# Kernel tuning notes

Measured on AMD Instinct MI355X. Metric: run time of the kernel, lower is better.

Reference implementation:

```python
import jax, jax.numpy as jnp
import numpy as np

N, T, K, V, E = 64, 256, 64, 32000, 100


def setup_inputs() -> dict:
    key = jax.random.key(0)
    ks = jax.random.split(key, 7)
    x = jax.random.randint(ks[0], (N, T), 0, V)
    emb_weight = jax.random.normal(ks[1], (V, E), dtype=jnp.float32)
    # trans: Linear(E, K*K, bias=False), weight uniform(-1,1)
    W_trans = jax.random.uniform(ks[2], (K * K, E), minval=-1.0, maxval=1.0, dtype=jnp.float32)
    # start: Linear(1, K)
    start_w = jax.random.normal(ks[3], (K, 1), dtype=jnp.float32) * 0.1
    start_b = jax.random.normal(ks[4], (K,), dtype=jnp.float32) * 0.1
    # emb_cluster: Embedding(K, K)
    emb_cluster_w = jax.random.normal(ks[5], (K, K), dtype=jnp.float32)
    # vocab: Linear(K, V, bias=False), weight uniform(-1,1)
    vocab_w = jax.random.uniform(ks[6], (V, K), minval=-1.0, maxval=1.0, dtype=jnp.float32)
    return {"x": x, "emb_weight": emb_weight, "W_trans": W_trans,
            "start_w": start_w, "start_b": start_b,
            "emb_cluster_w": emb_cluster_w, "vocab_w": vocab_w}


def reference(x, emb_weight, W_trans, start_w, start_b, emb_cluster_w, vocab_w):
    n, t = x.shape
    k = emb_cluster_w.shape[0]
    # word embeddings used to condition transitions at steps 0..T-2
    xe = emb_weight[x[:, :-1]]                                   # [N,T-1,E]
    # transition log-probs: log_softmax over destination state
    tran = jax.nn.log_softmax(
        jnp.einsum('nte,ce->ntc', xe, W_trans).reshape(n, t - 1, k, k), axis=-1)
    # emission log-probs per cluster: E[k, v]
    Elog = jax.nn.log_softmax(emb_cluster_w @ vocab_w.T, axis=-1)  # [K,V]
    emit = Elog.T[x[:, 1:]]                                       # [N,T-1,K]
    # initial alpha: log_softmax(start(ones)) expanded over batch
    alpha0 = jax.nn.log_softmax(start_w[:, 0] + start_b)           # [K]
    alpha0 = jnp.broadcast_to(alpha0[None, :], (n, k))
    tran_t = jnp.moveaxis(tran, 1, 0)   # [T-1,N,K,K]
    emit_t = jnp.moveaxis(emit, 1, 0)   # [T-1,N,K]

    def step(alpha, te):
        tr, em = te
        # logsumexp over previous state j: alpha[n,j] + tr[n,j,k]
        a = jax.scipy.special.logsumexp(alpha[:, :, None] + tr, axis=1) + em
        return a, None

    alpha, _ = jax.lax.scan(step, alpha0, (tran_t, emit_t))
    return -jnp.mean(jax.scipy.special.logsumexp(alpha, axis=1))
```

## Files before the change

kernel.cpp:

```cpp
#include <hip/hip_runtime.h>
#include <hip/hip_bf16.h>
#include <stdint.h>

#define NT 16320
#define NTPAD 16384
#define KDIM 128
#define NCOLS 4096
#define NSEQ 64
#define TSTEPS 255
#define VOCAB 32000
#define EDIM 100
#define CHUNKS 32
#define CLEN 8

typedef __attribute__((ext_vector_type(8))) short s8v;
typedef __attribute__((ext_vector_type(4))) float f4v;

__device__ __forceinline__ float bflo(uint32_t u) { return __uint_as_float(u << 16); }
__device__ __forceinline__ float bfhi(uint32_t u) { return __uint_as_float(u & 0xffff0000u); }

__device__ __forceinline__ void load_lds16(const void* g, void* l) {
    __builtin_amdgcn_global_load_lds(
        (const __attribute__((address_space(1))) void*)(uintptr_t)g,
        (__attribute__((address_space(3))) void*)(uintptr_t)l,
        16, 0, 0);
}

__global__ __launch_bounds__(256) void prep_dk(const int* __restrict__ x,
                                               const float* __restrict__ emb,
                                               const float* __restrict__ Wt,
                                               const float* __restrict__ ec,
                                               const float* __restrict__ vw,
                                               __hip_bfloat16* __restrict__ A,
                                               __hip_bfloat16* __restrict__ B,
                                               float* __restrict__ partials) {
    int bid = blockIdx.x;
    int tid = threadIdx.x;
    if (bid < 1280) {
        int rloc = tid >> 4, q = tid & 15;
        int b = bid * 16 + rloc;
        int c0 = q * 8;
        float vals[8] = {0.f, 0.f, 0.f, 0.f, 0.f, 0.f, 0.f, 0.f};
        __hip_bfloat16* dst;
        if (b < NTPAD) {
            if (b < NT) {
                int n = b / TSTEPS;
                int t = b - n * TSTEPS;
                int tok = x[n * 256 + t];
                const float* er = emb + (size_t)tok * EDIM;
#pragma unroll
                for (int i = 0; i < 8; ++i) { int e = c0 + i; if (e < EDIM) vals[i] = er[e]; }
            }
            dst = A + (size_t)b * KDIM + c0;
        } else {
            int cc = b - NTPAD;
            const float* wr = Wt + (size_t)cc * EDIM;
#pragma unroll
            for (int i = 0; i < 8; ++i) { int e = c0 + i; if (e < EDIM) vals[i] = wr[e]; }
            dst = B + (size_t)cc * KDIM + c0;
        }
        union { __hip_bfloat16 h[8]; uint4 u; } pk;
#pragma unroll
        for (int i = 0; i < 8; ++i) pk.h[i] = __float2bfloat16(vals[i]);
        *(uint4*)dst = pk.u;
    } else {
        int db = bid - 1280;
        int wave = tid >> 6, lane = tid & 63;
        float er[64];
        {
            const float4* ecv = (const float4*)(ec + (size_t)lane * 64);
#pragma unroll
            for (int i = 0; i < 16; ++i) {
                float4 v = ecv[i];
                er[4 * i] = v.x; er[4 * i + 1] = v.y; er[4 * i + 2] = v.z; er[4 * i + 3] = v.w;
            }
        }
        int v0 = db * 125;
        float m = -1e30f, s = 0.f;
        for (int v = v0 + wave; v < v0 + 125; v += 4) {
            int vu = __builtin_amdgcn_readfirstlane(v);
            const float* row = vw + (size_t)vu * 64;
            float acc = 0.f;
#pragma unroll
            for (int e = 0; e < 64; ++e) acc += er[e] * row[e];
            float nm = fmaxf(m, acc);
            s = s * __expf(m - nm) + __expf(acc - nm);
            m = nm;
        }
        __shared__ float pm[4][64], ps[4][64];
        pm[wave][lane] = m; ps[wave][lane] = s;
        __syncthreads();
        if (tid < 64) {
            float M = pm[0][tid], Ssum = ps[0][tid];
#pragma unroll
            for (int w = 1; w < 4; ++w) {
                float m2 = pm[w][tid], s2 = ps[w][tid];
                float nm = fmaxf(M, m2);
                Ssum = Ssum * __expf(M - nm) + s2 * __expf(m2 - nm);
                M = nm;
            }
            partials[(db * 64 + tid) * 2]     = M;
            partials[(db * 64 + tid) * 2 + 1] = Ssum;
        }
    }
}

__global__ __launch_bounds__(256) void dreduce(const float* __restrict__ partials,
                                               float* __restrict__ d) {
    __shared__ float pm[4][64], ps[4][64];
    int k = threadIdx.x & 63, part = threadIdx.x >> 6;
    float M = -1e30f, S = 0.f;
    for (int b = part; b < 256; b += 4) {
        float m2 = partials[(b * 64 + k) * 2];
        float s2 = partials[(b * 64 + k) * 2 + 1];
        float nm = fmaxf(M, m2);
        S = S * __expf(M - nm) + s2 * __expf(m2 - nm);
        M = nm;
    }
    pm[part][k] = M; ps[part][k] = S;
    __syncthreads();
    if (threadIdx.x < 64) {
        float Mm = pm[0][k], Ss = ps[0][k];
#pragma unroll
        for (int w = 1; w < 4; ++w) {
            float m2 = pm[w][k], s2 = ps[w][k];
            float nm = fmaxf(Mm, m2);
            Ss = Ss * __expf(Mm - nm) + s2 * __expf(m2 - nm);
            Mm = nm;
        }
        d[k] = Mm + __logf(Ss);
    }
}

__global__ __launch_bounds__(256) void emit_kern(const int* __restrict__ x,
                                                 const float* __restrict__ ec,
                                                 const float* __restrict__ vw,
                                                 const float* __restrict__ d,
                                                 __hip_bfloat16* __restrict__ emB) {
    int tid = threadIdx.x;
    int wave = tid >> 6, lane = tid & 63;
    float er[64];
    {
        const float4* ecv = (const float4*)(ec + (size_t)lane * 64);
#pragma unroll
        for (int i = 0; i < 16; ++i) {
            float4 v = ecv[i];
            er[4 * i] = v.x; er[4 * i + 1] = v.y; er[4 * i + 2] = v.z; er[4 * i + 3] = v.w;
        }
    }
    float dj = d[lane];
    int j = lane;
    int pos = ((j >> 2) & 3) * 16 + ((j >> 4) & 3) * 4 + (j & 3);
    int nt0 = blockIdx.x * 16 + wave * 4;
#pragma unroll
    for (int s = 0; s < 4; ++s) {
        int nt = nt0 + s;
        int n = nt / TSTEPS;
        int t = nt - n * TSTEPS;
        int tok = x[n * 256 + t + 1];
        tok = __builtin_amdgcn_readfirstlane(tok);
        const float* row = vw + (size_t)tok * 64;
        float acc = 0.f;
#pragma unroll
        for (int e = 0; e < 64; ++e) acc += er[e] * row[e];
        emB[(size_t)nt * 64 + pos] = __float2bfloat16(__expf(acc - dj));
    }
}

__global__ __launch_bounds__(256) void gemm_kern(const __hip_bfloat16* __restrict__ A,
                                                 const __hip_bfloat16* __restrict__ B,
                                                 const __hip_bfloat16* __restrict__ emB,
                                                 __hip_bfloat16* __restrict__ Eg) {
    int mblk = blockIdx.x;
    int nblk = blockIdx.y;
    int tid = threadIdx.x, wave = tid >> 6, lane = tid & 63;

    __shared__ __align__(16) char smem[65536];
    char* sA = smem;
    char* sB = smem + 32768;

    {
        int r0 = wave * 32;
        int l16 = lane & 15;
        int rsub = lane >> 4;
#pragma unroll
        for (int g = 0; g < 8; ++g) {
            int r = r0 + g * 4 + rsub;
            int chunk = l16 ^ (r & 7);
            const char* gp = (const char*)(A + (size_t)(mblk * 128 + r) * KDIM) + chunk * 16;
            load_lds16(gp, sA + (r0 + g * 4) * 256);
        }
#pragma unroll
        for (int g = 0; g < 8; ++g) {
            int c = r0 + g * 4 + rsub;
            int chunk = l16 ^ (c & 7);
            const char* gp = (const char*)(B + (size_t)(nblk * 128 + c) * KDIM) + chunk * 16;
            load_lds16(gp, sB + (r0 + g * 4) * 256);
        }
    }
    __syncthreads();

    int wc = (wave >> 1) * 64, wm = (wave & 1) * 64;
    int l15 = lane & 15, g4 = lane >> 4;
    f4v acc[4][4] = {};
#pragma unroll
    for (int k32 = 0; k32 < 4; ++k32) {
        s8v af[4], bf[4];
#pragma unroll
        for (int jt = 0; jt < 4; ++jt) {
            int r = wc + jt * 16 + l15;
            int chunk = (k32 * 4 + g4) ^ (r & 7);
            af[jt] = *(const s8v*)(sB + r * 256 + chunk * 16);
        }
#pragma unroll
        for (int mt = 0; mt < 4; ++mt) {
            int r = wm + mt * 16 + l15;
            int chunk = (k32 * 4 + g4) ^ (r & 7);
            bf[mt] = *(const s8v*)(sA + r * 256 + chunk * 16);
        }
#pragma unroll
        for (int jt = 0; jt < 4; ++jt)
#pragma unroll
            for (int mt = 0; mt < 4; ++mt)
                acc[jt][mt] = __builtin_amdgcn_mfma_f32_16x16x32_bf16(af[jt], bf[mt], acc[jt][mt], 0, 0, 0);
    }
    __syncthreads();

    char* sW = smem;
    const char* emb8 = (const char*)emB;
#pragma unroll
    for (int mt = 0; mt < 4; ++mt) {
        int mrow = wm + mt * 16 + l15;
        int mglob = mblk * 128 + mrow;
        float v[16];
#pragma unroll
        for (int jt = 0; jt < 4; ++jt)
#pragma unroll
            for (int rr = 0; rr < 4; ++rr) v[jt * 4 + rr] = acc[jt][mt][rr];
        float mx = v[0];
#pragma unroll
        for (int k = 1; k < 16; ++k) mx = fmaxf(mx, v[k]);
        mx = fmaxf(mx, __shfl_xor(mx, 16, 64));
        mx = fmaxf(mx, __shfl_xor(mx, 32, 64));
        float ex[16], sg = 0.f;
#pragma unroll
        for (int k = 0; k < 16; ++k) { ex[k] = __expf(v[k] - mx); sg += ex[k]; }
        sg += __shfl_xor(sg, 16, 64);
        sg += __shfl_xor(sg, 32, 64);
        float inv = 1.0f / sg;
        uint4 e0 = *(const uint4*)(emb8 + (size_t)mglob * 128 + g4 * 32);
        uint4 e1 = *(const uint4*)(emb8 + (size_t)mglob * 128 + g4 * 32 + 16);
        float em[16];
        {
            const uint32_t* w0 = (const uint32_t*)&e0;
            const uint32_t* w1 = (const uint32_t*)&e1;
#pragma unroll
            for (int i = 0; i < 4; ++i) {
                em[2 * i] = bflo(w0[i]);     em[2 * i + 1] = bfhi(w0[i]);
                em[8 + 2 * i] = bflo(w1[i]); em[8 + 2 * i + 1] = bfhi(w1[i]);
            }
        }
#pragma unroll
        for (int jt = 0; jt < 4; ++jt) {
            union { __hip_bfloat16 h[4]; uint2 u; } pk;
#pragma unroll
            for (int rr = 0; rr < 4; ++rr)
                pk.h[rr] = __float2bfloat16(ex[jt * 4 + rr] * inv * em[jt * 4 + rr]);
            *(uint2*)(sW + mrow * 272 + (wc + jt * 16 + g4 * 4) * 2) = pk.u;
        }
    }
    __syncthreads();

    {
        int rloc = tid >> 3;
        int q = tid & 7;
#pragma unroll
        for (int rp = 0; rp < 4; ++rp) {
            int row = rp * 32 + rloc;
            char* dst = (char*)Eg + (size_t)(mblk * 128 + row) * 8192 + nblk * 256;
            const char* src = sW + row * 272;
            *(uint4*)(dst + q * 16)       = *(const uint4*)(src + q * 16);
            *(uint4*)(dst + 128 + q * 16) = *(const uint4*)(src + 128 + q * 16);
        }
    }
}

__global__ __launch_bounds__(64) void chunk_kern(const __hip_bfloat16* __restrict__ Eg,
                                                 __hip_bfloat16* __restrict__ Gout,
                                                 float* __restrict__ Rout) {
    int lane = threadIdx.x;
    int l15 = lane & 15, g4 = lane >> 4;
    int id = blockIdx.x;
    int n = id >> 5;
    int c = id & 31;
    int base_m = n * TSTEPS + c * CLEN;
    int len = (c == 31) ? 7 : 8;

    __shared__ __align__(16) char sGT[64 * 144];

    {
        uint4 z = {0, 0, 0, 0};
#pragma unroll
        for (int i = 0; i < 8; ++i) *(uint4*)(sGT + lane * 144 + i * 16) = z;
        *(uint16_t*)(sGT + lane * 144 + lane * 2) = 0x3F80;
    }

    const char* Ebase = (const char*)Eg;
    uint4 pf[4][2];
    {
        const char* tp = Ebase + (size_t)(base_m + len - 1) * 8192;
#pragma unroll
        for (int at = 0; at < 4; ++at)
#pragma unroll
            for (int kk = 0; kk < 2; ++kk)
                pf[at][kk] = *(const uint4*)(tp + (at * 16 + l15) * 128 + kk * 64 + g4 * 16);
    }

    float rlog[4] = {0.f, 0.f, 0.f, 0.f};

    for (int tl = len - 1; tl >= 0; --tl) {
        uint4 af[4][2];
#pragma unroll
        for (int at = 0; at < 4; ++at) { af[at][0] = pf[at][0]; af[at][1] = pf[at][1]; }
        if (tl > 0) {
            const char* tp = Ebase + (size_t)(base_m + tl - 1) * 8192;
#pragma unroll
            for (int at = 0; at < 4; ++at)
#pragma unroll
                for (int kk = 0; kk < 2; ++kk)
                    pf[at][kk] = *(const uint4*)(tp + (at * 16 + l15) * 128 + kk * 64 + g4 * 16);
        }

        f4v acc[4][4] = {};
#pragma unroll
        for (int kk = 0; kk < 2; ++kk) {
#pragma unroll
            for (int ct = 0; ct < 4; ++ct) {
                s8v b = *(const s8v*)(sGT + (ct * 16 + l15) * 144 + kk * 64 + g4 * 16);
#pragma unroll
                for (int at = 0; at < 4; ++at)
                    acc[at][ct] = __builtin_amdgcn_mfma_f32_16x16x32_bf16(
                        *(const s8v*)&af[at][kk], b, acc[at][ct], 0, 0, 0);
            }
        }

#pragma unroll
        for (int ct = 0; ct < 4; ++ct) {
            float mx = acc[0][ct][0];
#pragma unroll
            for (int at = 0; at < 4; ++at)
#pragma unroll
                for (int rr = 0; rr < 4; ++rr) mx = fmaxf(mx, acc[at][ct][rr]);
            mx = fmaxf(mx, __shfl_xor(mx, 16, 64));
            mx = fmaxf(mx, __shfl_xor(mx, 32, 64));
            mx = fmaxf(mx, 1e-38f);
            rlog[ct] += __logf(mx);
            float inv = 1.0f / mx;
            int col = ct * 16 + l15;
#pragma unroll
            for (int at = 0; at < 4; ++at) {
                union { __hip_bfloat16 h[4]; uint2 u; } pk;
#pragma unroll
                for (int rr = 0; rr < 4; ++rr)
                    pk.h[rr] = __float2bfloat16(acc[at][ct][rr] * inv);
                *(uint2*)(sGT + col * 144 + at * 32 + g4 * 8) = pk.u;
            }
        }
    }

    {
        char* go = (char*)(Gout + (size_t)id * 4096 + lane * 64);
#pragma unroll
        for (int i = 0; i < 8; ++i)
            *(uint4*)(go + i * 16) = *(const uint4*)(sGT + lane * 144 + i * 16);
    }
    if (g4 == 0)
#pragma unroll
        for (int ct = 0; ct < 4; ++ct)
            Rout[(size_t)id * 64 + ct * 16 + l15] = rlog[ct];
}

__global__ __launch_bounds__(64) void combine_kern(const __hip_bfloat16* __restrict__ G,
                                                   const float* __restrict__ R,
                                                   const float* __restrict__ sw,
                                                   const float* __restrict__ sb,
                                                   float* __restrict__ out) {
    int n = blockIdx.x;
    int lane = threadIdx.x;
    __shared__ __align__(16) float sV[64];

    float alpha;
    {
        float v = sw[lane] + sb[lane];
        float m = v;
#pragma unroll
        for (int off = 1; off < 64; off <<= 1) m = fmaxf(m, __shfl_xor(m, off, 64));
        float s = __expf(v - m);
#pragma unroll
        for (int off = 1; off < 64; off <<= 1) s += __shfl_xor(s, off, 64);
        alpha = v - (m + __logf(s));
    }

    const char* Gb = (const char*)(G + (size_t)n * CHUNKS * 4096) + lane * 128;
    const float* Rb = R + (size_t)n * CHUNKS * 64 + lane;

    uint4 pf[8];
#pragma unroll
    for (int i = 0; i < 8; ++i) pf[i] = *(const uint4*)(Gb + i * 16);
    float rpf = Rb[0];

    for (int c = 0; c < CHUNKS; ++c) {
        uint4 cur[8];
#pragma unroll
        for (int i = 0; i < 8; ++i) cur[i] = pf[i];
        float rc = rpf;
        if (c + 1 < CHUNKS) {
            const char* gn = Gb + (size_t)(c + 1) * 8192;
#pragma unroll
            for (int i = 0; i < 8; ++i) pf[i] = *(const uint4*)(gn + i * 16);
            rpf = Rb[(c + 1) * 64];
        }

        float m = alpha;
#pragma unroll
        for (int off = 1; off < 64; off <<= 1) m = fmaxf(m, __shfl_xor(m, off, 64));
        sV[lane] = __expf(alpha - m);
        float acc = 0.f;
        const float4* sv4 = (const float4*)sV;
#pragma unroll
        for (int i = 0; i < 8; ++i) {
            const uint32_t* gw = (const uint32_t*)&cur[i];
            float4 va = sv4[2 * i], vb = sv4[2 * i + 1];
            acc += va.x * bflo(gw[0]) + va.y * bfhi(gw[0]);
            acc += va.z * bflo(gw[1]) + va.w * bfhi(gw[1]);
            acc += vb.x * bflo(gw[2]) + vb.y * bfhi(gw[2]);
            acc += vb.z * bflo(gw[3]) + vb.w * bfhi(gw[3]);
        }
        alpha = m + __logf(fmaxf(acc, 1e-38f)) + rc;
    }

    {
        float m = alpha;
#pragma unroll
        for (int off = 1; off < 64; off <<= 1) m = fmaxf(m, __shfl_xor(m, off, 64));
        float s = __expf(alpha - m);
#pragma unroll
        for (int off = 1; off < 64; off <<= 1) s += __shfl_xor(s, off, 64);
        if (lane == 0) atomicAdd(out, -(m + __logf(s)) * (1.0f / 64.0f));
    }
}

extern "C" void kernel_launch(void* const* d_in, const int* in_sizes, int n_in,
                              void* d_out, int out_size, void* d_ws, size_t ws_size,
                              hipStream_t stream) {
    const int*   x   = (const int*)d_in[0];
    const float* emb = (const float*)d_in[1];
    const float* Wt  = (const float*)d_in[2];
    const float* sw  = (const float*)d_in[3];
    const float* sb  = (const float*)d_in[4];
    const float* ec  = (const float*)d_in[5];
    const float* vw  = (const float*)d_in[6];
    float* out = (float*)d_out;
    char* ws = (char*)d_ws;

    __hip_bfloat16* Eg  = (__hip_bfloat16*)ws;
    __hip_bfloat16* A   = (__hip_bfloat16*)(ws + 134217728ull);
    __hip_bfloat16* B   = (__hip_bfloat16*)(ws + 138412032ull);
    __hip_bfloat16* emB = (__hip_bfloat16*)(ws + 139460608ull);
    float* dvec         = (float*)(ws + 141557760ull);
    float* partials     = (float*)(ws + 141558784ull);
    __hip_bfloat16* Gc  = (__hip_bfloat16*)(ws + 134217728ull);
    float* Rc           = (float*)(ws + 150994944ull);

    hipMemsetAsync(out, 0, sizeof(float), stream);

    prep_dk<<<1536, 256, 0, stream>>>(x, emb, Wt, ec, vw, A, B, partials);
    dreduce<<<1, 256, 0, stream>>>(partials, dvec);
    emit_kern<<<NT / 16, 256, 0, stream>>>(x, ec, vw, dvec, emB);
    gemm_kern<<<dim3(NTPAD / 128, NCOLS / 128), 256, 0, stream>>>(A, B, emB, Eg);
    chunk_kern<<<NSEQ * CHUNKS, 64, 0, stream>>>(Eg, Gc, Rc);
    combine_kern<<<NSEQ, 64, 0, stream>>>(Gc, Rc, sw, sb, out);
}
```

Baseline: 231.0 us.

## Narrow GEMM N-tile to 64 and rebalance scan chunks to 17x15

The GEMM now computes 128x64 output tiles instead of 128x128. This cuts LDS use and accumulator registers and doubles the number of blocks, which should raise occupancy. Stores for padded rows past NT are skipped. The chunked scan now splits each 255-step sequence into 17 chunks of exactly 15 steps instead of 32 chunks of 8, so every chunk has the same length and the combine stage has fewer chunks to merge, at the cost of fewer, longer chunk blocks. The Gc and Rc workspace buffers are moved to new offsets so they no longer overlap A and B.

```diff
diff --git a/kernel.cpp b/kernel.cpp
--- a/kernel.cpp
+++ b/kernel.cpp
@@ -10,8 +10,8 @@
 #define TSTEPS 255
 #define VOCAB 32000
 #define EDIM 100
-#define CHUNKS 32
-#define CLEN 8
+#define CHUNKS 17
+#define CLEN 15
 
 typedef __attribute__((ext_vector_type(8))) short s8v;
 typedef __attribute__((ext_vector_type(4))) float f4v;
@@ -175,45 +175,44 @@
     int nblk = blockIdx.y;
     int tid = threadIdx.x, wave = tid >> 6, lane = tid & 63;
 
-    __shared__ __align__(16) char smem[65536];
+    __shared__ __align__(16) char smem[49152];
     char* sA = smem;
     char* sB = smem + 32768;
 
     {
-        int r0 = wave * 32;
         int l16 = lane & 15;
         int rsub = lane >> 4;
 #pragma unroll
         for (int g = 0; g < 8; ++g) {
-            int r = r0 + g * 4 + rsub;
+            int r = wave * 32 + g * 4 + rsub;
             int chunk = l16 ^ (r & 7);
             const char* gp = (const char*)(A + (size_t)(mblk * 128 + r) * KDIM) + chunk * 16;
-            load_lds16(gp, sA + (r0 + g * 4) * 256);
-        }
-#pragma unroll
-        for (int g = 0; g < 8; ++g) {
-            int c = r0 + g * 4 + rsub;
-            int chunk = l16 ^ (c & 7);
-            const char* gp = (const char*)(B + (size_t)(nblk * 128 + c) * KDIM) + chunk * 16;
-            load_lds16(gp, sB + (r0 + g * 4) * 256);
+            load_lds16(gp, sA + (wave * 32 + g * 4) * 256);
+        }
+#pragma unroll
+        for (int g = 0; g < 4; ++g) {
+            int r = wave * 16 + g * 4 + rsub;
+            int chunk = l16 ^ (r & 7);
+            const char* gp = (const char*)(B + (size_t)(nblk * 64 + r) * KDIM) + chunk * 16;
+            load_lds16(gp, sB + (wave * 16 + g * 4) * 256);
         }
     }
     __syncthreads();
 
-    int wc = (wave >> 1) * 64, wm = (wave & 1) * 64;
+    int wm = wave * 32;
     int l15 = lane & 15, g4 = lane >> 4;
-    f4v acc[4][4] = {};
+    f4v acc[4][2] = {};
 #pragma unroll
     for (int k32 = 0; k32 < 4; ++k32) {
-        s8v af[4], bf[4];
+        s8v af[4], bf[2];
 #pragma unroll
         for (int jt = 0; jt < 4; ++jt) {
-            int r = wc + jt * 16 + l15;
+            int r = jt * 16 + l15;
             int chunk = (k32 * 4 + g4) ^ (r & 7);
             af[jt] = *(const s8v*)(sB + r * 256 + chunk * 16);
         }
 #pragma unroll
-        for (int mt = 0; mt < 4; ++mt) {
+        for (int mt = 0; mt < 2; ++mt) {
             int r = wm + mt * 16 + l15;
             int chunk = (k32 * 4 + g4) ^ (r & 7);
             bf[mt] = *(const s8v*)(sA + r * 256 + chunk * 16);
@@ -221,7 +220,7 @@
 #pragma unroll
         for (int jt = 0; jt < 4; ++jt)
 #pragma unroll
-            for (int mt = 0; mt < 4; ++mt)
+            for (int mt = 0; mt < 2; ++mt)
                 acc[jt][mt] = __builtin_amdgcn_mfma_f32_16x16x32_bf16(af[jt], bf[mt], acc[jt][mt], 0, 0, 0);
     }
     __syncthreads();
@@ -229,7 +228,7 @@
     char* sW = smem;
     const char* emb8 = (const char*)emB;
 #pragma unroll
-    for (int mt = 0; mt < 4; ++mt) {
+    for (int mt = 0; mt < 2; ++mt) {
         int mrow = wm + mt * 16 + l15;
         int mglob = mblk * 128 + mrow;
         float v[16];
@@ -266,21 +265,22 @@
 #pragma unroll
             for (int rr = 0; rr < 4; ++rr)
                 pk.h[rr] = __float2bfloat16(ex[jt * 4 + rr] * inv * em[jt * 4 + rr]);
-            *(uint2*)(sW + mrow * 272 + (wc + jt * 16 + g4 * 4) * 2) = pk.u;
+            *(uint2*)(sW + mrow * 136 + (jt * 16 + g4 * 4) * 2) = pk.u;
         }
     }
     __syncthreads();
 
     {
-        int rloc = tid >> 3;
-        int q = tid & 7;
+        int rloc = lane >> 3;
+        int q = lane & 7;
 #pragma unroll
         for (int rp = 0; rp < 4; ++rp) {
-            int row = rp * 32 + rloc;
-            char* dst = (char*)Eg + (size_t)(mblk * 128 + row) * 8192 + nblk * 256;
-            const char* src = sW + row * 272;
-            *(uint4*)(dst + q * 16)       = *(const uint4*)(src + q * 16);
-            *(uint4*)(dst + 128 + q * 16) = *(const uint4*)(src + 128 + q * 16);
+            int row = wave * 32 + rp * 8 + rloc;
+            int m = mblk * 128 + row;
+            if (m < NT) {
+                char* dst = (char*)Eg + (size_t)m * 8192 + nblk * 128;
+                *(uint4*)(dst + q * 16) = *(const uint4*)(sW + row * 136 + q * 16);
+            }
         }
     }
 }
@@ -291,10 +291,9 @@
     int lane = threadIdx.x;
     int l15 = lane & 15, g4 = lane >> 4;
     int id = blockIdx.x;
-    int n = id >> 5;
-    int c = id & 31;
+    int n = (id * 3856) >> 16;
+    int c = id - n * 17;
     int base_m = n * TSTEPS + c * CLEN;
-    int len = (c == 31) ? 7 : 8;
 
     __shared__ __align__(16) char sGT[64 * 144];
 
@@ -308,7 +307,7 @@
     const char* Ebase = (const char*)Eg;
     uint4 pf[4][2];
     {
-        const char* tp = Ebase + (size_t)(base_m + len - 1) * 8192;
+        const char* tp = Ebase + (size_t)(base_m + 14) * 8192;
 #pragma unroll
         for (int at = 0; at < 4; ++at)
 #pragma unroll
@@ -318,7 +317,7 @@
 
     float rlog[4] = {0.f, 0.f, 0.f, 0.f};
 
-    for (int tl = len - 1; tl >= 0; --tl) {
+    for (int tl = 14; tl >= 0; --tl) {
         uint4 af[4][2];
 #pragma unroll
         for (int at = 0; at < 4; ++at) { af[at][0] = pf[at][0]; af[at][1] = pf[at][1]; }
@@ -469,15 +468,15 @@
     __hip_bfloat16* emB = (__hip_bfloat16*)(ws + 139460608ull);
     float* dvec         = (float*)(ws + 141557760ull);
     float* partials     = (float*)(ws + 141558784ull);
-    __hip_bfloat16* Gc  = (__hip_bfloat16*)(ws + 134217728ull);
-    float* Rc           = (float*)(ws + 150994944ull);
+    __hip_bfloat16* Gc  = (__hip_bfloat16*)(ws + 141689856ull);
+    float* Rc           = (float*)(ws + 150602752ull);
 
     hipMemsetAsync(out, 0, sizeof(float), stream);
 
     prep_dk<<<1536, 256, 0, stream>>>(x, emb, Wt, ec, vw, A, B, partials);
     dreduce<<<1, 256, 0, stream>>>(partials, dvec);
     emit_kern<<<NT / 16, 256, 0, stream>>>(x, ec, vw, dvec, emB);
-    gemm_kern<<<dim3(NTPAD / 128, NCOLS / 128), 256, 0, stream>>>(A, B, emB, Eg);
+    gemm_kern<<<dim3(NTPAD / 128, NCOLS / 64), 256, 0, stream>>>(A, B, emB, Eg);
     chunk_kern<<<NSEQ * CHUNKS, 64, 0, stream>>>(Eg, Gc, Rc);
     combine_kern<<<NSEQ, 64, 0, stream>>>(Gc, Rc, sw, sb, out);
 }
```

After: 222.3 us. 1.04x faster.

## Fold dreduce into emit kernel, drop memset, use 17 chunks of 15 steps

Applied to the files above, without the earlier changes.

Removes the single-block dreduce launch by having each emit block redundantly reduce the partials into shared memory, and doubles per-block work in emit_kern. Replaces the hipMemsetAsync by zeroing the output inside chunk_kern. Changes the chunked scan to 17 chunks of 15 steps with renormalisation only every third step, cutting launches and per-step max/log work but risking bf16 range issues between rescales and adding redundant partial reductions in every emit block.

```diff
diff --git a/kernel.cpp b/kernel.cpp
--- a/kernel.cpp
+++ b/kernel.cpp
@@ -10,8 +10,8 @@
 #define TSTEPS 255
 #define VOCAB 32000
 #define EDIM 100
-#define CHUNKS 32
-#define CLEN 8
+#define CHUNKS 17
+#define CLEN 15
 
 typedef __attribute__((ext_vector_type(8))) short s8v;
 typedef __attribute__((ext_vector_type(4))) float f4v;
@@ -105,40 +105,27 @@
     }
 }
 
-__global__ __launch_bounds__(256) void dreduce(const float* __restrict__ partials,
-                                               float* __restrict__ d) {
-    __shared__ float pm[4][64], ps[4][64];
-    int k = threadIdx.x & 63, part = threadIdx.x >> 6;
-    float M = -1e30f, S = 0.f;
-    for (int b = part; b < 256; b += 4) {
-        float m2 = partials[(b * 64 + k) * 2];
-        float s2 = partials[(b * 64 + k) * 2 + 1];
-        float nm = fmaxf(M, m2);
-        S = S * __expf(M - nm) + s2 * __expf(m2 - nm);
-        M = nm;
-    }
-    pm[part][k] = M; ps[part][k] = S;
-    __syncthreads();
-    if (threadIdx.x < 64) {
-        float Mm = pm[0][k], Ss = ps[0][k];
-#pragma unroll
-        for (int w = 1; w < 4; ++w) {
-            float m2 = pm[w][k], s2 = ps[w][k];
-            float nm = fmaxf(Mm, m2);
-            Ss = Ss * __expf(Mm - nm) + s2 * __expf(m2 - nm);
-            Mm = nm;
-        }
-        d[k] = Mm + __logf(Ss);
-    }
-}
-
 __global__ __launch_bounds__(256) void emit_kern(const int* __restrict__ x,
                                                  const float* __restrict__ ec,
                                                  const float* __restrict__ vw,
-                                                 const float* __restrict__ d,
+                                                 const float* __restrict__ partials,
                                                  __hip_bfloat16* __restrict__ emB) {
+    __shared__ float pm[4][64], ps[4][64], sD[64];
     int tid = threadIdx.x;
     int wave = tid >> 6, lane = tid & 63;
+
+    {
+        float M = -1e30f, S = 0.f;
+        for (int b = wave; b < 256; b += 4) {
+            float m2 = partials[(b * 64 + lane) * 2];
+            float s2 = partials[(b * 64 + lane) * 2 + 1];
+            float nm = fmaxf(M, m2);
+            S = S * __expf(M - nm) + s2 * __expf(m2 - nm);
+            M = nm;
+        }
+        pm[wave][lane] = M; ps[wave][lane] = S;
+    }
+
     float er[64];
     {
         const float4* ecv = (const float4*)(ec + (size_t)lane * 64);
@@ -148,12 +135,26 @@
             er[4 * i] = v.x; er[4 * i + 1] = v.y; er[4 * i + 2] = v.z; er[4 * i + 3] = v.w;
         }
     }
-    float dj = d[lane];
+    __syncthreads();
+    if (tid < 64) {
+        float M = pm[0][tid], S = ps[0][tid];
+#pragma unroll
+        for (int w = 1; w < 4; ++w) {
+            float m2 = pm[w][tid], s2 = ps[w][tid];
+            float nm = fmaxf(M, m2);
+            S = S * __expf(M - nm) + s2 * __expf(m2 - nm);
+            M = nm;
+        }
+        sD[tid] = M + __logf(S);
+    }
+    __syncthreads();
+
+    float dj = sD[lane];
     int j = lane;
     int pos = ((j >> 2) & 3) * 16 + ((j >> 4) & 3) * 4 + (j & 3);
-    int nt0 = blockIdx.x * 16 + wave * 4;
-#pragma unroll
-    for (int s = 0; s < 4; ++s) {
+    int nt0 = blockIdx.x * 32 + wave * 8;
+#pragma unroll
+    for (int s = 0; s < 8; ++s) {
         int nt = nt0 + s;
         int n = nt / TSTEPS;
         int t = nt - n * TSTEPS;
@@ -287,14 +288,15 @@
 
 __global__ __launch_bounds__(64) void chunk_kern(const __hip_bfloat16* __restrict__ Eg,
                                                  __hip_bfloat16* __restrict__ Gout,
-                                                 float* __restrict__ Rout) {
+                                                 float* __restrict__ Rout,
+                                                 float* __restrict__ out) {
     int lane = threadIdx.x;
+    if (blockIdx.x == 0 && lane == 0) *out = 0.f;
     int l15 = lane & 15, g4 = lane >> 4;
     int id = blockIdx.x;
-    int n = id >> 5;
-    int c = id & 31;
+    int n = (id * 3856) >> 16;
+    int c = id - n * 17;
     int base_m = n * TSTEPS + c * CLEN;
-    int len = (c == 31) ? 7 : 8;
 
     __shared__ __align__(16) char sGT[64 * 144];
 
@@ -308,7 +310,7 @@
     const char* Ebase = (const char*)Eg;
     uint4 pf[4][2];
     {
-        const char* tp = Ebase + (size_t)(base_m + len - 1) * 8192;
+        const char* tp = Ebase + (size_t)(base_m + 14) * 8192;
 #pragma unroll
         for (int at = 0; at < 4; ++at)
 #pragma unroll
@@ -318,7 +320,7 @@
 
     float rlog[4] = {0.f, 0.f, 0.f, 0.f};
 
-    for (int tl = len - 1; tl >= 0; --tl) {
+    for (int tl = 14; tl >= 0; --tl) {
         uint4 af[4][2];
 #pragma unroll
         for (int at = 0; at < 4; ++at) { af[at][0] = pf[at][0]; af[at][1] = pf[at][1]; }
@@ -344,26 +346,41 @@
             }
         }
 
-#pragma unroll
-        for (int ct = 0; ct < 4; ++ct) {
-            float mx = acc[0][ct][0];
-#pragma unroll
-            for (int at = 0; at < 4; ++at)
-#pragma unroll
-                for (int rr = 0; rr < 4; ++rr) mx = fmaxf(mx, acc[at][ct][rr]);
-            mx = fmaxf(mx, __shfl_xor(mx, 16, 64));
-            mx = fmaxf(mx, __shfl_xor(mx, 32, 64));
-            mx = fmaxf(mx, 1e-38f);
-            rlog[ct] += __logf(mx);
-            float inv = 1.0f / mx;
-            int col = ct * 16 + l15;
-#pragma unroll
-            for (int at = 0; at < 4; ++at) {
-                union { __hip_bfloat16 h[4]; uint2 u; } pk;
-#pragma unroll
-                for (int rr = 0; rr < 4; ++rr)
-                    pk.h[rr] = __float2bfloat16(acc[at][ct][rr] * inv);
-                *(uint2*)(sGT + col * 144 + at * 32 + g4 * 8) = pk.u;
+        if (tl % 3 == 0) {
+#pragma unroll
+            for (int ct = 0; ct < 4; ++ct) {
+                float mx = acc[0][ct][0];
+#pragma unroll
+                for (int at = 0; at < 4; ++at)
+#pragma unroll
+                    for (int rr = 0; rr < 4; ++rr) mx = fmaxf(mx, acc[at][ct][rr]);
+                mx = fmaxf(mx, __shfl_xor(mx, 16, 64));
+                mx = fmaxf(mx, __shfl_xor(mx, 32, 64));
+                mx = fmaxf(mx, 1e-38f);
+                rlog[ct] += __logf(mx);
+                float inv = 1.0f / mx;
+                int col = ct * 16 + l15;
+#pragma unroll
+                for (int at = 0; at < 4; ++at) {
+                    union { __hip_bfloat16 h[4]; uint2 u; } pk;
+#pragma unroll
+                    for (int rr = 0; rr < 4; ++rr)
+                        pk.h[rr] = __float2bfloat16(acc[at][ct][rr] * inv);
+                    *(uint2*)(sGT + col * 144 + at * 32 + g4 * 8) = pk.u;
+                }
+            }
+        } else {
+#pragma unroll
+            for (int ct = 0; ct < 4; ++ct) {
+                int col = ct * 16 + l15;
+#pragma unroll
+                for (int at = 0; at < 4; ++at) {
+                    union { __hip_bfloat16 h[4]; uint2 u; } pk;
+#pragma unroll
+                    for (int rr = 0; rr < 4; ++rr)
+                        pk.h[rr] = __float2bfloat16(acc[at][ct][rr]);
+                    *(uint2*)(sGT + col * 144 + at * 32 + g4 * 8) = pk.u;
+                }
             }
         }
     }
@@ -467,17 +484,13 @@
     __hip_bfloat16* A   = (__hip_bfloat16*)(ws + 134217728ull);
     __hip_bfloat16* B   = (__hip_bfloat16*)(ws + 138412032ull);
     __hip_bfloat16* emB = (__hip_bfloat16*)(ws + 139460608ull);
-    float* dvec         = (float*)(ws + 141557760ull);
-    float* partials     = (float*)(ws + 141558784ull);
-    __hip_bfloat16* Gc  = (__hip_bfloat16*)(ws + 134217728ull);
-    float* Rc           = (float*)(ws + 150994944ull);
-
-    hipMemsetAsync(out, 0, sizeof(float), stream);
+    float* partials     = (float*)(ws + 141557760ull);
+    __hip_bfloat16* Gc  = (__hip_bfloat16*)(ws + 141688832ull);
+    float* Rc           = (float*)(ws + 150601728ull);
 
     prep_dk<<<1536, 256, 0, stream>>>(x, emb, Wt, ec, vw, A, B, partials);
-    dreduce<<<1, 256, 0, stream>>>(partials, dvec);
-    emit_kern<<<NT / 16, 256, 0, stream>>>(x, ec, vw, dvec, emB);
+    emit_kern<<<510, 256, 0, stream>>>(x, ec, vw, partials, emB);
     gemm_kern<<<dim3(NTPAD / 128, NCOLS / 128), 256, 0, stream>>>(A, B, emB, Eg);
-    chunk_kern<<<NSEQ * CHUNKS, 64, 0, stream>>>(Eg, Gc, Rc);
+    chunk_kern<<<NSEQ * CHUNKS, 64, 0, stream>>>(Eg, Gc, Rc, out);
     combine_kern<<<NSEQ, 64, 0, stream>>>(Gc, Rc, sw, sb, out);
 }
```

Measured after the change: 213.7 us. -7.5%, faster.
